# Kernel tuning notes

Measured on AMD Instinct MI355X. Metric: run time of the kernel, lower is better.

Reference implementation:

```python
import jax, jax.numpy as jnp
import numpy as np

TAU_FF = 10
TAU_FB = 10
NB_FF = 8
NB_FB = 1
MU = 0.5
N_IN = 2048
N_HID = 2048
N_OUT = 2048


def raised_cosine_pillow_08(tau, n_basis, mu):
    # Pillow et al. 2008 log-raised-cosine basis; returns [n_basis, tau].
    # Fixed (non-learned) constant in the original module.
    t = jnp.arange(tau, dtype=jnp.float32)
    c = jnp.arange(n_basis, dtype=jnp.float32)
    arg = jnp.clip(mu * jnp.pi * jnp.log1p(t)[None, :] - mu * jnp.pi * c[:, None],
                   -jnp.pi, jnp.pi)
    return 0.5 * (1.0 + jnp.cos(arg))


# transposed like the torch module: [tau, n_basis]
FF_FILT = raised_cosine_pillow_08(TAU_FF, NB_FF, MU).T
FB_FILT = raised_cosine_pillow_08(TAU_FB, NB_FB, MU).T


def _layer_step(inp_hist, spk_hist, ff_w, fb_w, bias, key):
    # inp_hist: [n_in, T]; spk_hist: [n_out, Th]; ff_w: [n_out, n_in, NB_FF]
    T = inp_hist.shape[-1]
    ff_trace = jnp.matmul(inp_hist[..., ::-1], FF_FILT[:T])       # [n_in, NB_FF]
    ff_pot = jnp.einsum('oib,ib->o', ff_w, ff_trace)              # [n_out]
    Th = spk_hist.shape[-1]
    fb_trace = jnp.matmul(spk_hist[:, ::-1], FB_FILT[:Th])        # [n_out, NB_FB]
    fb_pot = jnp.sum(fb_w * fb_trace, axis=-1)                    # [n_out]
    p = jax.nn.sigmoid(ff_pot + fb_pot + bias)
    spikes = jax.random.bernoulli(key, jax.lax.stop_gradient(p)).astype(p.dtype)
    # memory_length (10) > current history width (2), so the update just
    # appends one column (matches torch slice [:, 1-memory_length:]).
    new_hist = jnp.concatenate([spk_hist, spikes[:, None]], axis=-1)
    return p, spikes, new_hist


def setup_inputs() -> dict:
    key = jax.random.key(0)
    ks = jax.random.split(key, 10)

    def xav(k, shape, fan_in, fan_out):
        a = np.sqrt(3.0) * np.sqrt(2.0 / float(fan_in + fan_out))
        return jax.random.uniform(k, shape, jnp.float32, -a, a)

    fi, fo = N_IN * NB_FF, N_HID * NB_FF  # fan of ff_weights [n_out, n_in, nb]
    return {
        'inputs_history': (jax.random.uniform(ks[0], (N_IN, TAU_FF)) < 0.3).astype(jnp.float32),
        'ff_w0': xav(ks[1], (N_HID, N_IN, NB_FF), fi, fo),
        'fb_w0': xav(ks[2], (N_HID, NB_FB), fi, fo),
        'b0': xav(ks[3], (N_HID,), fi, fo),
        'ff_w1': xav(ks[4], (N_HID, N_HID, NB_FF), fi, fo),
        'fb_w1': xav(ks[5], (N_HID, NB_FB), fi, fo),
        'b1': xav(ks[6], (N_HID,), fi, fo),
        'ff_w2': xav(ks[7], (N_OUT, N_HID, NB_FF), fi, fo),
        'fb_w2': xav(ks[8], (N_OUT, NB_FB), fi, fo),
        'b2': xav(ks[9], (N_OUT,), fi, fo),
    }


def reference(inputs_history, ff_w0, fb_w0, b0, ff_w1, fb_w1, b1,
              ff_w2, fb_w2, b2):
    # LayeredSNN.forward with n_samples=1, target=None.
    k0, k1, k2 = jax.random.split(jax.random.key(42), 3)
    h0 = jnp.zeros((N_HID, 2), jnp.float32)   # initial spiking histories
    h1 = jnp.zeros((N_HID, 2), jnp.float32)
    h2 = jnp.zeros((N_OUT, 2), jnp.float32)
    p0, s0, h0 = _layer_step(inputs_history, h0, ff_w0, fb_w0, b0, k0)
    p1, s1, h1 = _layer_step(h0, h1, ff_w1, fb_w1, b1, k1)   # reads updated h0
    p2, s2, h2 = _layer_step(h1, h2, ff_w2, fb_w2, b2, k2)   # out layer
    net_probas = p2[None]                      # [1, n_out]
    net_outputs = s2[None]                     # [1, n_out]
    probas_hidden = jnp.stack([p0, p1])[None]  # [1, n_hidden_layers, n_hid]
    outputs_hidden = jnp.stack([s0, s1])[None]
    return net_probas, net_outputs, probas_hidden, outputs_hidden
```

## Files before the change

kernel.cpp:

```cpp
#include <hip/hip_runtime.h>
#include <hip/hip_bf16.h>
#include <stdint.h>
#include <stddef.h>

#define WS_F_OFF      64
#define WS_TRACE0_OFF 768
#define WS_S0_OFF     131840
#define WS_S1_OFF     148224

__host__ __device__ inline void tf2x32(uint32_t k0, uint32_t k1,
                                       uint32_t& x0, uint32_t& x1) {
  uint32_t ks0 = k0, ks1 = k1, ks2 = k0 ^ k1 ^ 0x1BD11BDAu;
  x0 += ks0; x1 += ks1;
#define TF_ROT(v, n) (((v) << (n)) | ((v) >> (32 - (n))))
#define TF_R(r) { x0 += x1; x1 = TF_ROT(x1, r); x1 ^= x0; }
  TF_R(13) TF_R(15) TF_R(26) TF_R(6)   x0 += ks1; x1 += ks2 + 1u;
  TF_R(17) TF_R(29) TF_R(16) TF_R(24)  x0 += ks2; x1 += ks0 + 2u;
  TF_R(13) TF_R(15) TF_R(26) TF_R(6)   x0 += ks0; x1 += ks1 + 3u;
  TF_R(17) TF_R(29) TF_R(16) TF_R(24)  x0 += ks1; x1 += ks2 + 4u;
  TF_R(13) TF_R(15) TF_R(26) TF_R(6)   x0 += ks2; x1 += ks0 + 5u;
#undef TF_R
#undef TF_ROT
}

__device__ inline double bf2d(unsigned short b) {
  return (double)__uint_as_float(((uint32_t)b) << 16);
}
__device__ inline unsigned short f2bf(float f) {
  uint32_t u = __float_as_uint(f);
  u += 0x7FFFu + ((u >> 16) & 1u);
  return (unsigned short)(u >> 16);
}

__global__ __launch_bounds__(256) void snn_prep_kernel(
    const void* __restrict__ X, uint8_t* __restrict__ ws) {
  __shared__ unsigned long long smask[4];
  __shared__ double sF[80];
  __shared__ int s_flag;
  const int tid = threadIdx.x;

  const uint32_t* xw = (const uint32_t*)X;
  uint32_t w = xw[tid];
  bool ok = (w == 0u || w == 0x3F800000u);
  unsigned long long m = __ballot(ok);
  if ((tid & 63) == 0) smask[tid >> 6] = m;

  if (tid < 80) {
    int tt = tid >> 3, b = tid & 7;
    const double PI = 3.14159265358979311599796346854;
    double arg = 0.5 * PI * log1p((double)tt) - 0.5 * PI * (double)b;
    arg = fmin(fmax(arg, -PI), PI);
    sF[tid] = 0.5 * (1.0 + cos(arg));
  }
  __syncthreads();
  if (tid == 0) {
    bool allbin = ((smask[0] & smask[1] & smask[2] & smask[3]) == ~0ull);
    s_flag = allbin ? 0 : 1;
  }
  __syncthreads();
  const int flag = s_flag;

  if (blockIdx.x == 0) {
    if (tid == 0) *(uint32_t*)ws = (uint32_t)flag;
    if (tid < 80) ((double*)(ws + WS_F_OFF))[tid] = sF[tid];
  }

  const int idx = blockIdx.x * 256 + tid;
  const int i = idx >> 3, b = idx & 7;
  double acc = 0.0;
  if (flag) {
    const unsigned short* Xb = (const unsigned short*)X;
    #pragma unroll
    for (int t = 0; t < 10; ++t) acc += bf2d(Xb[i * 10 + (9 - t)]) * sF[t * 8 + b];
  } else {
    const float* Xf = (const float*)X;
    #pragma unroll
    for (int t = 0; t < 10; ++t) acc += (double)Xf[i * 10 + (9 - t)] * sF[t * 8 + b];
  }
  ((double*)(ws + WS_TRACE0_OFF))[idx] = acc;
}

__global__ __launch_bounds__(256) void snn_layer_kernel(
    const void* __restrict__ W, const void* __restrict__ bias,
    const uint8_t* __restrict__ ws,
    int traceMode,
    const double* __restrict__ sPrev,
    double* __restrict__ sOutD,
    uint32_t key0, uint32_t key1,
    void* __restrict__ out, int pOff, int sOff)
{
  const uint32_t flag = *(const uint32_t*)ws;
  const double* F = (const double*)(ws + WS_F_OFF);
  const double* tr0 = (const double*)(ws + WS_TRACE0_OFF);
  const int lane = threadIdx.x & 63;
  const int row = blockIdx.x * 4 + (threadIdx.x >> 6);

  double acc[8];
  #pragma unroll
  for (int b = 0; b < 8; ++b) acc[b] = 0.0;

  if (traceMode == 0) {
    if (flag) {
      const unsigned short* Wr = (const unsigned short*)W + (size_t)row * 16384;
      for (int s = 0; s < 32; ++s) {
        int i = s * 64 + lane;
        uint4 v = *(const uint4*)(Wr + i * 8);
        const double2* t = (const double2*)(tr0 + i * 8);
        double2 t0 = t[0], t1 = t[1], t2 = t[2], t3 = t[3];
        acc[0] += bf2d((unsigned short)(v.x & 0xFFFFu)) * t0.x;
        acc[1] += bf2d((unsigned short)(v.x >> 16))     * t0.y;
        acc[2] += bf2d((unsigned short)(v.y & 0xFFFFu)) * t1.x;
        acc[3] += bf2d((unsigned short)(v.y >> 16))     * t1.y;
        acc[4] += bf2d((unsigned short)(v.z & 0xFFFFu)) * t2.x;
        acc[5] += bf2d((unsigned short)(v.z >> 16))     * t2.y;
        acc[6] += bf2d((unsigned short)(v.w & 0xFFFFu)) * t3.x;
        acc[7] += bf2d((unsigned short)(v.w >> 16))     * t3.y;
      }
    } else {
      const float* Wr = (const float*)W + (size_t)row * 16384;
      for (int s = 0; s < 32; ++s) {
        int i = s * 64 + lane;
        float4 a = *(const float4*)(Wr + i * 8);
        float4 c = *(const float4*)(Wr + i * 8 + 4);
        const double2* t = (const double2*)(tr0 + i * 8);
        double2 t0 = t[0], t1 = t[1], t2 = t[2], t3 = t[3];
        acc[0] += (double)a.x * t0.x;  acc[1] += (double)a.y * t0.y;
        acc[2] += (double)a.z * t1.x;  acc[3] += (double)a.w * t1.y;
        acc[4] += (double)c.x * t2.x;  acc[5] += (double)c.y * t2.y;
        acc[6] += (double)c.z * t3.x;  acc[7] += (double)c.w * t3.y;
      }
    }
  } else {
    double F0[8];
    #pragma unroll
    for (int b = 0; b < 8; ++b) F0[b] = F[b];
    if (flag) {
      const unsigned short* Wr = (const unsigned short*)W + (size_t)row * 16384;
      for (int s = 0; s < 32; ++s) {
        int i = s * 64 + lane;
        uint4 v = *(const uint4*)(Wr + i * 8);
        double si = sPrev[i];
        acc[0] += (bf2d((unsigned short)(v.x & 0xFFFFu)) * F0[0]) * si;
        acc[1] += (bf2d((unsigned short)(v.x >> 16))     * F0[1]) * si;
        acc[2] += (bf2d((unsigned short)(v.y & 0xFFFFu)) * F0[2]) * si;
        acc[3] += (bf2d((unsigned short)(v.y >> 16))     * F0[3]) * si;
        acc[4] += (bf2d((unsigned short)(v.z & 0xFFFFu)) * F0[4]) * si;
        acc[5] += (bf2d((unsigned short)(v.z >> 16))     * F0[5]) * si;
        acc[6] += (bf2d((unsigned short)(v.w & 0xFFFFu)) * F0[6]) * si;
        acc[7] += (bf2d((unsigned short)(v.w >> 16))     * F0[7]) * si;
      }
    } else {
      const float* Wr = (const float*)W + (size_t)row * 16384;
      for (int s = 0; s < 32; ++s) {
        int i = s * 64 + lane;
        float4 a = *(const float4*)(Wr + i * 8);
        float4 c = *(const float4*)(Wr + i * 8 + 4);
        double si = sPrev[i];
        acc[0] += ((double)a.x * F0[0]) * si;
        acc[1] += ((double)a.y * F0[1]) * si;
        acc[2] += ((double)a.z * F0[2]) * si;
        acc[3] += ((double)a.w * F0[3]) * si;
        acc[4] += ((double)c.x * F0[4]) * si;
        acc[5] += ((double)c.y * F0[5]) * si;
        acc[6] += ((double)c.z * F0[6]) * si;
        acc[7] += ((double)c.w * F0[7]) * si;
      }
    }
  }

  double r = ((acc[0] + acc[1]) + (acc[2] + acc[3])) +
             ((acc[4] + acc[5]) + (acc[6] + acc[7]));
  #pragma unroll
  for (int off = 32; off > 0; off >>= 1) r += __shfl_down(r, off, 64);

  if (lane == 0) {
    double bb = flag ? bf2d(((const unsigned short*)bias)[row])
                     : (double)((const float*)bias)[row];
    double x = r + bb;
    double p = 1.0 / (1.0 + exp(-x));
    uint32_t x0 = 0u, x1 = (uint32_t)row;
    tf2x32(key0, key1, x0, x1);
    uint32_t wbits = x0 ^ x1;
    float u = __uint_as_float((wbits >> 9) | 0x3F800000u) - 1.0f;
    double sp = ((double)u < p) ? 1.0 : 0.0;
    if (flag) {
      unsigned short* ob = (unsigned short*)out;
      ob[pOff + row] = f2bf((float)p);
      ob[sOff + row] = f2bf((float)sp);
    } else {
      float* of = (float*)out;
      of[pOff + row] = (float)p;
      of[sOff + row] = (float)sp;
    }
    if (sOutD) sOutD[row] = sp;
  }
}

extern "C" void kernel_launch(void* const* d_in, const int* in_sizes, int n_in,
                              void* d_out, int out_size, void* d_ws, size_t ws_size,
                              hipStream_t stream) {
  uint32_t k0a = 0u, k0b = 0u;  tf2x32(0u, 42u, k0a, k0b);
  uint32_t k1a = 0u, k1b = 1u;  tf2x32(0u, 42u, k1a, k1b);
  uint32_t k2a = 0u, k2b = 2u;  tf2x32(0u, 42u, k2a, k2b);

  uint8_t* ws = (uint8_t*)d_ws;
  double* s0d = (double*)(ws + WS_S0_OFF);
  double* s1d = (double*)(ws + WS_S1_OFF);

  snn_prep_kernel<<<64, 256, 0, stream>>>(d_in[0], ws);
  snn_layer_kernel<<<512, 256, 0, stream>>>(d_in[1], d_in[3], ws, 0, nullptr, s0d,
                                            k0a, k0b, d_out, 4096, 8192);
  snn_layer_kernel<<<512, 256, 0, stream>>>(d_in[4], d_in[6], ws, 1, s0d, s1d,
                                            k1a, k1b, d_out, 6144, 10240);
  snn_layer_kernel<<<512, 256, 0, stream>>>(d_in[7], d_in[9], ws, 1, s1d, nullptr,
                                            k2a, k2b, d_out, 0, 2048);
}
```

Measured before the change: 376.5 us.

## Split each output row across two waves and transpose trace layout

Each output row is now reduced by two wavefronts, each covering half of the input dimension, and the partial sums are combined through shared memory. The grid doubles to 1024 blocks, which gives more waves in flight to hide the latency of streaming the weight matrices. The layer-0 trace is stored basis-major so per-basis loads coalesce across lanes, and the inner loops are unrolled by four. The cost is an extra block-wide barrier and a shared-memory combine per row.

Result: no change. 373.4 us (-0.8%).

```diff
diff --git a/kernel.cpp b/kernel.cpp
--- a/kernel.cpp
+++ b/kernel.cpp
@@ -77,7 +77,7 @@
     #pragma unroll
     for (int t = 0; t < 10; ++t) acc += (double)Xf[i * 10 + (9 - t)] * sF[t * 8 + b];
   }
-  ((double*)(ws + WS_TRACE0_OFF))[idx] = acc;
+  ((double*)(ws + WS_TRACE0_OFF))[b * 2048 + i] = acc;
 }
 
 __global__ __launch_bounds__(256) void snn_layer_kernel(
@@ -91,9 +91,12 @@
 {
   const uint32_t flag = *(const uint32_t*)ws;
   const double* F = (const double*)(ws + WS_F_OFF);
-  const double* tr0 = (const double*)(ws + WS_TRACE0_OFF);
+  const double* trT = (const double*)(ws + WS_TRACE0_OFF);
   const int lane = threadIdx.x & 63;
-  const int row = blockIdx.x * 4 + (threadIdx.x >> 6);
+  const int wid  = threadIdx.x >> 6;
+  const int row  = blockIdx.x * 2 + (wid >> 1);
+  const int half = wid & 1;
+  const int ibase = half * 1024;
 
   double acc[8];
   #pragma unroll
@@ -102,32 +105,34 @@
   if (traceMode == 0) {
     if (flag) {
       const unsigned short* Wr = (const unsigned short*)W + (size_t)row * 16384;
-      for (int s = 0; s < 32; ++s) {
-        int i = s * 64 + lane;
+      #pragma unroll 4
+      for (int s = 0; s < 16; ++s) {
+        int i = ibase + s * 64 + lane;
         uint4 v = *(const uint4*)(Wr + i * 8);
-        const double2* t = (const double2*)(tr0 + i * 8);
-        double2 t0 = t[0], t1 = t[1], t2 = t[2], t3 = t[3];
-        acc[0] += bf2d((unsigned short)(v.x & 0xFFFFu)) * t0.x;
-        acc[1] += bf2d((unsigned short)(v.x >> 16))     * t0.y;
-        acc[2] += bf2d((unsigned short)(v.y & 0xFFFFu)) * t1.x;
-        acc[3] += bf2d((unsigned short)(v.y >> 16))     * t1.y;
-        acc[4] += bf2d((unsigned short)(v.z & 0xFFFFu)) * t2.x;
-        acc[5] += bf2d((unsigned short)(v.z >> 16))     * t2.y;
-        acc[6] += bf2d((unsigned short)(v.w & 0xFFFFu)) * t3.x;
-        acc[7] += bf2d((unsigned short)(v.w >> 16))     * t3.y;
+        acc[0] += bf2d((unsigned short)(v.x & 0xFFFFu)) * trT[0 * 2048 + i];
+        acc[1] += bf2d((unsigned short)(v.x >> 16))     * trT[1 * 2048 + i];
+        acc[2] += bf2d((unsigned short)(v.y & 0xFFFFu)) * trT[2 * 2048 + i];
+        acc[3] += bf2d((unsigned short)(v.y >> 16))     * trT[3 * 2048 + i];
+        acc[4] += bf2d((unsigned short)(v.z & 0xFFFFu)) * trT[4 * 2048 + i];
+        acc[5] += bf2d((unsigned short)(v.z >> 16))     * trT[5 * 2048 + i];
+        acc[6] += bf2d((unsigned short)(v.w & 0xFFFFu)) * trT[6 * 2048 + i];
+        acc[7] += bf2d((unsigned short)(v.w >> 16))     * trT[7 * 2048 + i];
       }
     } else {
       const float* Wr = (const float*)W + (size_t)row * 16384;
-      for (int s = 0; s < 32; ++s) {
-        int i = s * 64 + lane;
+      #pragma unroll 4
+      for (int s = 0; s < 16; ++s) {
+        int i = ibase + s * 64 + lane;
         float4 a = *(const float4*)(Wr + i * 8);
         float4 c = *(const float4*)(Wr + i * 8 + 4);
-        const double2* t = (const double2*)(tr0 + i * 8);
-        double2 t0 = t[0], t1 = t[1], t2 = t[2], t3 = t[3];
-        acc[0] += (double)a.x * t0.x;  acc[1] += (double)a.y * t0.y;
-        acc[2] += (double)a.z * t1.x;  acc[3] += (double)a.w * t1.y;
-        acc[4] += (double)c.x * t2.x;  acc[5] += (double)c.y * t2.y;
-        acc[6] += (double)c.z * t3.x;  acc[7] += (double)c.w * t3.y;
+        acc[0] += (double)a.x * trT[0 * 2048 + i];
+        acc[1] += (double)a.y * trT[1 * 2048 + i];
+        acc[2] += (double)a.z * trT[2 * 2048 + i];
+        acc[3] += (double)a.w * trT[3 * 2048 + i];
+        acc[4] += (double)c.x * trT[4 * 2048 + i];
+        acc[5] += (double)c.y * trT[5 * 2048 + i];
+        acc[6] += (double)c.z * trT[6 * 2048 + i];
+        acc[7] += (double)c.w * trT[7 * 2048 + i];
       }
     }
   } else {
@@ -136,8 +141,9 @@
     for (int b = 0; b < 8; ++b) F0[b] = F[b];
     if (flag) {
       const unsigned short* Wr = (const unsigned short*)W + (size_t)row * 16384;
-      for (int s = 0; s < 32; ++s) {
-        int i = s * 64 + lane;
+      #pragma unroll 4
+      for (int s = 0; s < 16; ++s) {
+        int i = ibase + s * 64 + lane;
         uint4 v = *(const uint4*)(Wr + i * 8);
         double si = sPrev[i];
         acc[0] += (bf2d((unsigned short)(v.x & 0xFFFFu)) * F0[0]) * si;
@@ -151,8 +157,9 @@
       }
     } else {
       const float* Wr = (const float*)W + (size_t)row * 16384;
-      for (int s = 0; s < 32; ++s) {
-        int i = s * 64 + lane;
+      #pragma unroll 4
+      for (int s = 0; s < 16; ++s) {
+        int i = ibase + s * 64 + lane;
         float4 a = *(const float4*)(Wr + i * 8);
         float4 c = *(const float4*)(Wr + i * 8 + 4);
         double si = sPrev[i];
@@ -173,26 +180,32 @@
   #pragma unroll
   for (int off = 32; off > 0; off >>= 1) r += __shfl_down(r, off, 64);
 
-  if (lane == 0) {
-    double bb = flag ? bf2d(((const unsigned short*)bias)[row])
-                     : (double)((const float*)bias)[row];
-    double x = r + bb;
+  __shared__ double sred[4];
+  if (lane == 0) sred[wid] = r;
+  __syncthreads();
+
+  if (threadIdx.x < 2) {
+    const int o = blockIdx.x * 2 + threadIdx.x;
+    double rr = sred[2 * threadIdx.x] + sred[2 * threadIdx.x + 1];
+    double bb = flag ? bf2d(((const unsigned short*)bias)[o])
+                     : (double)((const float*)bias)[o];
+    double x = rr + bb;
     double p = 1.0 / (1.0 + exp(-x));
-    uint32_t x0 = 0u, x1 = (uint32_t)row;
+    uint32_t x0 = 0u, x1 = (uint32_t)o;
     tf2x32(key0, key1, x0, x1);
     uint32_t wbits = x0 ^ x1;
     float u = __uint_as_float((wbits >> 9) | 0x3F800000u) - 1.0f;
     double sp = ((double)u < p) ? 1.0 : 0.0;
     if (flag) {
       unsigned short* ob = (unsigned short*)out;
-      ob[pOff + row] = f2bf((float)p);
-      ob[sOff + row] = f2bf((float)sp);
+      ob[pOff + o] = f2bf((float)p);
+      ob[sOff + o] = f2bf((float)sp);
     } else {
       float* of = (float*)out;
-      of[pOff + row] = (float)p;
-      of[sOff + row] = (float)sp;
+      of[pOff + o] = (float)p;
+      of[sOff + o] = (float)sp;
     }
-    if (sOutD) sOutD[row] = sp;
+    if (sOutD) sOutD[o] = sp;
   }
 }
 
@@ -208,10 +221,10 @@
   double* s1d = (double*)(ws + WS_S1_OFF);
 
   snn_prep_kernel<<<64, 256, 0, stream>>>(d_in[0], ws);
-  snn_layer_kernel<<<512, 256, 0, stream>>>(d_in[1], d_in[3], ws, 0, nullptr, s0d,
-                                            k0a, k0b, d_out, 4096, 8192);
-  snn_layer_kernel<<<512, 256, 0, stream>>>(d_in[4], d_in[6], ws, 1, s0d, s1d,
-                                            k1a, k1b, d_out, 6144, 10240);
-  snn_layer_kernel<<<512, 256, 0, stream>>>(d_in[7], d_in[9], ws, 1, s1d, nullptr,
-                                            k2a, k2b, d_out, 0, 2048);
-}
+  snn_layer_kernel<<<1024, 256, 0, stream>>>(d_in[1], d_in[3], ws, 0, nullptr, s0d,
+                                             k0a, k0b, d_out, 4096, 8192);
+  snn_layer_kernel<<<1024, 256, 0, stream>>>(d_in[4], d_in[6], ws, 1, s0d, s1d,
+                                             k1a, k1b, d_out, 6144, 10240);
+  snn_layer_kernel<<<1024, 256, 0, stream>>>(d_in[7], d_in[9], ws, 1, s1d, nullptr,
+                                             k2a, k2b, d_out, 0, 2048);
+}
```
